# Kernel tuning notes

Hardware: AMD Instinct MI355X
Metric: run time of the kernel (lower is better)

The kernel has to match this reference:

```python
import jax, jax.numpy as jnp
import numpy as np

ALPHA = 1.0
MIN_FEATURE_SIZE = 1.0
SC = 1e-12                      # stabilizer added to first derivatives
EPS_V_FLOOR = 1e-32 / 6.0       # torch.tensor(1e-32 ** 1 / 6) == 1e-32/6 (** binds tighter than /)


def _grad2d(phi, d):
    """Vectorized equivalent of numerical_gradient_2d: central differences in the
    interior, one-sided forward/backward differences at the boundaries."""
    gx = jnp.concatenate([
        (phi[1:2, :] - phi[0:1, :]) / d,           # forward diff at i == 0
        (phi[2:, :] - phi[:-2, :]) / (2.0 * d),    # central diff in interior
        (phi[-1:, :] - phi[-2:-1, :]) / d,         # backward diff at i == H-1
    ], axis=0)
    gy = jnp.concatenate([
        (phi[:, 1:2] - phi[:, 0:1]) / d,
        (phi[:, 2:] - phi[:, :-2]) / (2.0 * d),
        (phi[:, -1:] - phi[:, -2:-1]) / d,
    ], axis=1)
    return gx, gy


def setup_inputs() -> dict:
    key = jax.random.key(0)
    eps = jax.random.normal(key, (4096, 4096), dtype=jnp.float32)
    grid_size = jnp.asarray(0.05, dtype=jnp.float32)
    return {"eps": eps, "grid_size": grid_size}


def reference(eps, grid_size):
    # mirror the field along axis 1 (torch.cat((eps, eps.flip(1)), dim=1)) -> [H, 2W]
    eps = jnp.concatenate([eps, eps[:, ::-1]], axis=1)

    # ls_derivatives: first derivatives (+SC), then second derivatives of those
    eps_x, eps_y = _grad2d(eps, grid_size)
    eps_x = eps_x + SC
    eps_y = eps_y + SC
    eps_xx, eps_xy = _grad2d(eps_x, grid_size)
    _, eps_yy = _grad2d(eps_y, grid_size)

    pi_d = np.pi / (1.1 * MIN_FEATURE_SIZE)
    eps_v = jnp.maximum(jnp.sqrt(eps_x**2 + eps_y**2), EPS_V_FLOOR)
    k = (eps_x**2 * eps_yy - 2.0 * eps_x * eps_y * eps_xy + eps_y**2 * eps_xx) / eps_v**3
    curve_const = jnp.abs(k * jnp.arctan(eps_v / eps)) - pi_d
    return jnp.nansum(ALPHA * jnp.maximum(curve_const, 0.0) * grid_size**2)
```

## Files before the change

### kernel.cpp

```cpp
#include <hip/hip_runtime.h>
#include <math.h>


#define BLOCK_X 256
#define ROWS_PER 32

typedef float f32x2 __attribute__((ext_vector_type(2)));

__device__ __forceinline__ f32x2 mk2(float a, float b) { f32x2 v; v.x = a; v.y = b; return v; }
__device__ __forceinline__ f32x2 sp2(float a) { return mk2(a, a); }

#if __has_builtin(__builtin_elementwise_fma)
__device__ __forceinline__ f32x2 fma2(f32x2 a, f32x2 b, f32x2 c) { return __builtin_elementwise_fma(a, b, c); }
#else
__device__ __forceinline__ f32x2 fma2(f32x2 a, f32x2 b, f32x2 c) { return mk2(fmaf(a.x, b.x, c.x), fmaf(a.y, b.y, c.y)); }
#endif
#if __has_builtin(__builtin_elementwise_max)
__device__ __forceinline__ f32x2 max2(f32x2 a, f32x2 b) { return __builtin_elementwise_max(a, b); }
#else
__device__ __forceinline__ f32x2 max2(f32x2 a, f32x2 b) { return mk2(fmaxf(a.x, b.x), fmaxf(a.y, b.y)); }
#endif
__device__ __forceinline__ f32x2 abs2(f32x2 a) { return mk2(fabsf(a.x), fabsf(a.y)); }


__device__ __forceinline__ float fast_atan_ratio(float v, float c, float rv)
{
    const float rc = __builtin_amdgcn_rcpf(c);
    const float q  = v * rc;
    const float iq = c * rv;
    const bool  big = fabsf(q) > 1.0f;
    const float t  = big ? iq : q;
    const float s  = t * t;
    float p = fmaf(s, -0.01172120f, 0.05265332f);
    p = fmaf(s, p, -0.11643287f);
    p = fmaf(s, p,  0.19354346f);
    p = fmaf(s, p, -0.33262347f);
    p = fmaf(s, p,  0.99997726f);
    const float at = p * t;
    const float hp = copysignf(1.57079632679f, q);
    return big ? (hp - at) : at;
}

__device__ __forceinline__ f32x2 fast_atan_ratio2(f32x2 v, f32x2 c, f32x2 rvv)
{
    const f32x2 rc = mk2(__builtin_amdgcn_rcpf(c.x), __builtin_amdgcn_rcpf(c.y));
    const f32x2 q  = v * rc;
    const f32x2 iq = c * rvv;
    const bool big0 = fabsf(q.x) > 1.0f, big1 = fabsf(q.y) > 1.0f;
    const f32x2 t = mk2(big0 ? iq.x : q.x, big1 ? iq.y : q.y);
    const f32x2 s = t * t;
    f32x2 p = fma2(s, sp2(-0.01172120f), sp2(0.05265332f));
    p = fma2(s, p, sp2(-0.11643287f));
    p = fma2(s, p, sp2( 0.19354346f));
    p = fma2(s, p, sp2(-0.33262347f));
    p = fma2(s, p, sp2( 0.99997726f));
    const f32x2 at = p * t;
    const float hp0 = copysignf(1.57079632679f, q.x);
    const float hp1 = copysignf(1.57079632679f, q.y);
    return mk2(big0 ? (hp0 - at.x) : at.x, big1 ? (hp1 - at.y) : at.y);
}

template<bool XE>
__device__ __forceinline__ void load6(const float* __restrict__ rowp, int j0,
                                      bool left, bool right,
                                      f32x2& m, f32x2& c, f32x2& p)
{
    c = *reinterpret_cast<const f32x2*>(rowp + j0);
    if (XE) {
        const float* ma = rowp + (left  ? j0 : j0 - 2);
        const float* pa = rowp + (right ? j0 : j0 + 2);
        m = *reinterpret_cast<const f32x2*>(ma);
        p = *reinterpret_cast<const f32x2*>(pa);
        if (left)  m = mk2(c.x, c.x);
        if (right) p = mk2(c.y, c.x);
    } else {
        m = *reinterpret_cast<const f32x2*>(rowp + j0 - 2);
        p = *reinterpret_cast<const f32x2*>(rowp + j0 + 2);
    }
}

template<bool XE>
__device__ __forceinline__ f32x2 strip_packed(
    const float* __restrict__ eps, int Wn, int i0, int j0,
    bool left, bool right, float rd2, f32x2 syjv, f32x2 symv)
{
    const f32x2 SC2    = sp2(1e-12f);
    const float FLOORV = (float)(1e-32 / 6.0);
    const float pi_d   = 3.14159265358979323846f / 1.1f;
    const f32x2 rd2v   = sp2(rd2);
    const f32x2 sxy    = syjv * rd2;

    const float* r0 = eps + (size_t)(i0 - 2) * (size_t)Wn;
    const f32x2 Ac = *reinterpret_cast<const f32x2*>(r0 + j0);
    f32x2 Bm, Bc, Bp, Cm, Cc, Cp, Dm, Dc, Dp, Em, Ec, Ep;
    load6<XE>(r0 + (size_t)Wn,     j0, left, right, Bm, Bc, Bp);
    load6<XE>(r0 + (size_t)2 * Wn, j0, left, right, Cm, Cc, Cp);
    load6<XE>(r0 + (size_t)3 * Wn, j0, left, right, Dm, Dc, Dp);
    load6<XE>(r0 + (size_t)4 * Wn, j0, left, right, Em, Ec, Ep);
    const float* pr = r0 + (size_t)5 * Wn;

    f32x2 xm1 = fma2(Cc - Ac, rd2v, SC2);
    f32x2 gc0 = Dc - Bc;
    f32x2 x0  = fma2(gc0, rd2v, SC2);
    f32x2 gc1 = Ec - Cc;
    f32x2 xp1 = fma2(gc1, rd2v, SC2);

    f32x2 acc = sp2(0.0f);
    #pragma unroll 4
    for (int r = 0; r < ROWS_PER; ++r) {
        f32x2 Fm, Fc, Fp;
        load6<XE>(pr, j0, left, right, Fm, Fc, Fp);
        pr += Wn;

        const f32x2 gc2 = Fc - Dc;
        const f32x2 x2v = fma2(gc2, rd2v, SC2);

        const f32x2 ex  = x0;
        const f32x2 exx = (xp1 - xm1) * rd2;
        const f32x2 Cl1 = mk2(Cm.y, Cc.x), Cr1 = mk2(Cc.y, Cp.x);
        const f32x2 ey  = fma2(Cr1 - Cl1, syjv, SC2);
        f32x2 eyw = fma2(Cc - Cm, symv, SC2);
        const f32x2 eye = fma2(Cp - Cc, rd2v, SC2);
        if (XE) { if (left) eyw.x = ey.x; }
        const f32x2 eyy = (eye - eyw) * syjv;
        const f32x2 Gm = Dm - Bm, Gp = Dp - Bp;
        const f32x2 exyL = mk2(Gm.y, gc0.x), exyR = mk2(gc0.y, Gp.x);
        const f32x2 exy = (exyR - exyL) * sxy;

        const f32x2 t1 = ex * ex, t2 = ey * ey;
        f32x2 num = t1 * eyy;
        num = fma2(t2, exx, num);
        num = fma2((ex * ey) * -2.0f, exy, num);
        const f32x2 ssum = t1 + t2;
        const f32x2 rvv = mk2(__builtin_amdgcn_rsqf(ssum.x),
                              __builtin_amdgcn_rsqf(ssum.y));
        f32x2 evv = ssum * rvv;
        evv = max2(evv, sp2(FLOORV));
        const f32x2 k   = num * (rvv * rvv) * rvv;
        const f32x2 at  = fast_atan_ratio2(evv, Cc, rvv);
        const f32x2 cc  = abs2(k * at) - sp2(pi_d);
        acc = acc + max2(cc, sp2(0.0f));

        xm1 = x0; x0 = xp1; xp1 = x2v; gc0 = gc1; gc1 = gc2;
        Bm = Cm; Bp = Cp;
        Cm = Dm; Cc = Dc; Cp = Dp;
        Dm = Em; Dc = Ec; Dp = Ep;
        Em = Fm; Ec = Fc; Ep = Fp;
    }
    (void)Bc;
    return acc;
}

__device__ float strip_scalar_yb(const float* __restrict__ eps, int Hn, int Wn,
                                 int i0, int j, float rd, float rd2)
{
    const float SC     = 1e-12f;
    const float FLOORV = (float)(1e-32 / 6.0);
    const float pi_d   = 3.14159265358979323846f / 1.1f;

    const int jm  = (j > 0) ? j - 1 : 0;
    const int jmm = (j > 1) ? j - 2 : 0;
    const int jp = j + 1, jpp = j + 2;
    const int cjp  = (jp  < Wn) ? jp  : (2 * Wn - 1 - jp);
    const int cjpp = (jpp < Wn) ? jpp : (2 * Wn - 1 - jpp);
    const bool jz = (j == 0);
    const float syj = jz ? rd : rd2;
    const float sym = (jm == 0) ? rd : rd2;

    auto rp = [&](int t) -> const float* {
        int tt = t < 0 ? 0 : t;
        tt = tt > Hn - 1 ? Hn - 1 : tt;
        return eps + (size_t)tt * (size_t)Wn;
    };

    float a2 = rp(i0 - 2)[j],   a1 = rp(i0 - 1)[j],  a0 = rp(i0)[j];
    float b1 = rp(i0 + 1)[j],   b2 = rp(i0 + 2)[j];
    float wN = rp(i0 - 1)[jm],  w0 = rp(i0)[jm],     wS = rp(i0 + 1)[jm];
    float eN = rp(i0 - 1)[cjp], e0 = rp(i0)[cjp],    eS = rp(i0 + 1)[cjp];
    float ww = rp(i0)[jmm],     ee = rp(i0)[cjpp];

    float acc = 0.0f;
    #pragma unroll 4
    for (int r = 0; r < ROWS_PER; ++r) {
        const int i = i0 + r;
        const float* q3 = rp(i + 3);
        const float* q2 = rp(i + 2);
        const float* q1 = rp(i + 1);
        const float nb2 = q3[j], nwS = q2[jm], neS = q2[cjp];
        const float nww = q1[jmm], nee = q1[cjpp];

        const bool itop = (i == 0), ibot = (i == Hn - 1);
        const float sxi = (itop || ibot) ? rd : rd2;
        const float sxm = (i == 1) ? rd : rd2;
        const float sxp = (i == Hn - 2) ? rd : rd2;

        const float ex = fmaf(b1 - a1, sxi, SC);
        const float ey = fmaf(e0 - w0, syj, SC);
        float exn = fmaf(a0 - a2, sxm, SC);
        float exs = fmaf(b2 - a0, sxp, SC);
        if (itop) exn = ex;
        if (ibot) exs = ex;
        const float exx = (exs - exn) * sxi;
        float eyw = fmaf(a0 - ww, sym, SC);
        const float eye = fmaf(ee - a0, rd2, SC);
        if (jz) eyw = ey;
        const float eyy = (eye - eyw) * syj;
        const float exy = ((eS - eN) - (wS - wN)) * (sxi * syj);

        const float t1 = ex * ex, t2 = ey * ey;
        float num = t1 * eyy;
        num = fmaf(t2, exx, num);
        num = fmaf(-2.0f * (ex * ey), exy, num);
        const float ssum = t1 + t2;
        const float rv = __builtin_amdgcn_rsqf(ssum);
        float ev = ssum * rv;
        ev = fmaxf(ev, FLOORV);
        const float k  = num * (rv * rv) * rv;
        const float at = fast_atan_ratio(ev, a0, rv);
        const float ccv = fabsf(k * at) - pi_d;
        float contrib = fmaxf(ccv, 0.0f);
        if (i >= Hn) contrib = 0.0f;
        acc += contrib;

        a2 = a1; a1 = a0; a0 = b1; b1 = b2; b2 = nb2;
        wN = w0; w0 = wS; wS = nwS;
        eN = e0; e0 = eS; eS = neS;
        ww = nww; ee = nee;
    }
    return acc;
}

__global__ __launch_bounds__(BLOCK_X, 4) void curve_partial_kernel(
    const float* __restrict__ eps, const float* __restrict__ gs,
    double* __restrict__ partial, int Hn, int Wn)
{
    const int tx = threadIdx.x;
    const int j0 = (blockIdx.x * BLOCK_X + tx) * 2;
    const int i0 = blockIdx.y * ROWS_PER;
    const float d   = gs[0];
    const float rd  = 1.0f / d;
    const float rd2 = 0.5f * rd;
    const bool left  = (j0 == 0);
    const bool right = (j0 + 2 == Wn);

    const bool yint = (i0 >= 2) && (i0 + ROWS_PER + 2 < Hn);

    f32x2 accv;
    if (yint) {
        const f32x2 syjv = left ? mk2(rd,  rd2) : sp2(rd2);
        const f32x2 symv = left ? mk2(rd2, rd ) : sp2(rd2);
        const bool xe = (blockIdx.x == 0) || (blockIdx.x == gridDim.x - 1);
        accv = xe
            ? strip_packed<true >(eps, Wn, i0, j0, left, right, rd2, syjv, symv)
            : strip_packed<false>(eps, Wn, i0, j0, left, right, rd2, syjv, symv);
    } else {
        accv.x = strip_scalar_yb(eps, Hn, Wn, i0, j0,     rd, rd2);
        accv.y = strip_scalar_yb(eps, Hn, Wn, i0, j0 + 1, rd, rd2);
    }

    double acc = (double)accv.x + (double)accv.y;
    #pragma unroll
    for (int off = 32; off > 0; off >>= 1)
        acc += __shfl_down(acc, off, 64);
    __shared__ double lds[BLOCK_X / 64];
    const int lane = tx & 63, wv = tx >> 6;
    if (lane == 0) lds[wv] = acc;
    __syncthreads();
    if (tx == 0) {
        partial[blockIdx.y * gridDim.x + blockIdx.x] =
            lds[0] + lds[1] + lds[2] + lds[3];
    }
}

__global__ __launch_bounds__(256) void curve_finish_kernel(
    const double* __restrict__ partial, int n,
    const float* __restrict__ gs, float* __restrict__ out)
{
    const int tx = threadIdx.x;
    double acc = 0.0;
    for (int idx = tx; idx < n; idx += 256) acc += partial[idx];
    #pragma unroll
    for (int off = 32; off > 0; off >>= 1)
        acc += __shfl_down(acc, off, 64);
    __shared__ double lds[4];
    const int lane = tx & 63, wv = tx >> 6;
    if (lane == 0) lds[wv] = acc;
    __syncthreads();
    if (tx == 0) {
        const double dd = (double)gs[0];
        out[0] = (float)((lds[0] + lds[1] + lds[2] + lds[3]) * 2.0 * dd * dd);
    }
}

extern "C" void kernel_launch(void* const* d_in, const int* in_sizes, int n_in,
                              void* d_out, int out_size, void* d_ws, size_t ws_size,
                              hipStream_t stream) {
    const float* eps = (const float*)d_in[0];
    const float* gs  = (const float*)d_in[1];
    float* out = (float*)d_out;

    const int n = in_sizes[0];
    int Wn = (int)(sqrt((double)n) + 0.5);
    int Hn = n / Wn;

    const int gx = Wn / (BLOCK_X * 2);
    const int gy = (Hn + ROWS_PER - 1) / ROWS_PER;
    const int nb = gx * gy;
    double* partial = (double*)d_ws;

    curve_partial_kernel<<<dim3(gx, gy), BLOCK_X, 0, stream>>>(eps, gs, partial, Hn, Wn);
    curve_finish_kernel<<<1, 256, 0, stream>>>(partial, nb, gs, out);
}
```

Measured before the change: 108.6 us.

## Process four columns per thread with 16-byte loads and branch-light atan

```diff
diff --git a/kernel.cpp b/kernel.cpp
--- a/kernel.cpp
+++ b/kernel.cpp
@@ -3,9 +3,10 @@
 
 
 #define BLOCK_X 256
-#define ROWS_PER 32
+#define ROWS_PER 16
 
 typedef float f32x2 __attribute__((ext_vector_type(2)));
+typedef float f32x4 __attribute__((ext_vector_type(4)));
 
 __device__ __forceinline__ f32x2 mk2(float a, float b) { f32x2 v; v.x = a; v.y = b; return v; }
 __device__ __forceinline__ f32x2 sp2(float a) { return mk2(a, a); }
@@ -17,11 +18,49 @@
 #endif
 #if __has_builtin(__builtin_elementwise_max)
 __device__ __forceinline__ f32x2 max2(f32x2 a, f32x2 b) { return __builtin_elementwise_max(a, b); }
+__device__ __forceinline__ f32x2 min2(f32x2 a, f32x2 b) { return __builtin_elementwise_min(a, b); }
 #else
 __device__ __forceinline__ f32x2 max2(f32x2 a, f32x2 b) { return mk2(fmaxf(a.x, b.x), fmaxf(a.y, b.y)); }
+__device__ __forceinline__ f32x2 min2(f32x2 a, f32x2 b) { return mk2(fminf(a.x, b.x), fminf(a.y, b.y)); }
 #endif
 __device__ __forceinline__ f32x2 abs2(f32x2 a) { return mk2(fabsf(a.x), fabsf(a.y)); }
-
+__device__ __forceinline__ f32x2 rcp2(f32x2 a) { return mk2(__builtin_amdgcn_rcpf(a.x), __builtin_amdgcn_rcpf(a.y)); }
+
+struct V4 { f32x2 lo, hi; };
+__device__ __forceinline__ V4 mkv(f32x2 lo, f32x2 hi) { V4 r; r.lo = lo; r.hi = hi; return r; }
+__device__ __forceinline__ V4 splat4(float x) { return mkv(sp2(x), sp2(x)); }
+__device__ __forceinline__ V4 add4(V4 a, V4 b) { return mkv(a.lo + b.lo, a.hi + b.hi); }
+__device__ __forceinline__ V4 sub4(V4 a, V4 b) { return mkv(a.lo - b.lo, a.hi - b.hi); }
+__device__ __forceinline__ V4 mul4(V4 a, V4 b) { return mkv(a.lo * b.lo, a.hi * b.hi); }
+__device__ __forceinline__ V4 muls(V4 a, float s) { return mkv(a.lo * s, a.hi * s); }
+__device__ __forceinline__ V4 fma4(V4 a, V4 b, V4 c) { return mkv(fma2(a.lo, b.lo, c.lo), fma2(a.hi, b.hi, c.hi)); }
+__device__ __forceinline__ V4 fmas(V4 a, f32x2 s, f32x2 c) { return mkv(fma2(a.lo, s, c), fma2(a.hi, s, c)); }
+__device__ __forceinline__ V4 max4(V4 a, V4 b) { return mkv(max2(a.lo, b.lo), max2(a.hi, b.hi)); }
+__device__ __forceinline__ V4 abs4(V4 a) { return mkv(abs2(a.lo), abs2(a.hi)); }
+
+__device__ __forceinline__ V4 atan4_bl(V4 v, V4 c)
+{
+    V4 a  = abs4(c);
+    V4 mn = mkv(min2(v.lo, a.lo), min2(v.hi, a.hi));
+    V4 mx = mkv(max2(v.lo, a.lo), max2(v.hi, a.hi));
+    V4 r  = mkv(rcp2(mx.lo), rcp2(mx.hi));
+    V4 t  = mul4(mn, r);
+    V4 s  = mul4(t, t);
+    V4 p  = fma4(s, splat4(-0.01172120f), splat4(0.05265332f));
+    p = fma4(s, p, splat4(-0.11643287f));
+    p = fma4(s, p, splat4( 0.19354346f));
+    p = fma4(s, p, splat4(-0.33262347f));
+    p = fma4(s, p, splat4( 0.99997726f));
+    V4 at0 = mul4(p, t);
+    const f32x2 P2 = sp2(1.57079632679f);
+    V4 alt = mkv(P2 - at0.lo, P2 - at0.hi);
+    V4 res;
+    res.lo.x = copysignf((v.lo.x > a.lo.x) ? alt.lo.x : at0.lo.x, c.lo.x);
+    res.lo.y = copysignf((v.lo.y > a.lo.y) ? alt.lo.y : at0.lo.y, c.lo.y);
+    res.hi.x = copysignf((v.hi.x > a.hi.x) ? alt.hi.x : at0.hi.x, c.hi.x);
+    res.hi.y = copysignf((v.hi.y > a.hi.y) ? alt.hi.y : at0.hi.y, c.hi.y);
+    return res;
+}
 
 __device__ __forceinline__ float fast_atan_ratio(float v, float c, float rv)
 {
@@ -41,113 +80,117 @@
     return big ? (hp - at) : at;
 }
 
-__device__ __forceinline__ f32x2 fast_atan_ratio2(f32x2 v, f32x2 c, f32x2 rvv)
-{
-    const f32x2 rc = mk2(__builtin_amdgcn_rcpf(c.x), __builtin_amdgcn_rcpf(c.y));
-    const f32x2 q  = v * rc;
-    const f32x2 iq = c * rvv;
-    const bool big0 = fabsf(q.x) > 1.0f, big1 = fabsf(q.y) > 1.0f;
-    const f32x2 t = mk2(big0 ? iq.x : q.x, big1 ? iq.y : q.y);
-    const f32x2 s = t * t;
-    f32x2 p = fma2(s, sp2(-0.01172120f), sp2(0.05265332f));
-    p = fma2(s, p, sp2(-0.11643287f));
-    p = fma2(s, p, sp2( 0.19354346f));
-    p = fma2(s, p, sp2(-0.33262347f));
-    p = fma2(s, p, sp2( 0.99997726f));
-    const f32x2 at = p * t;
-    const float hp0 = copysignf(1.57079632679f, q.x);
-    const float hp1 = copysignf(1.57079632679f, q.y);
-    return mk2(big0 ? (hp0 - at.x) : at.x, big1 ? (hp1 - at.y) : at.y);
-}
+struct Row { f32x2 m, c0, c1, p; };
 
 template<bool XE>
-__device__ __forceinline__ void load6(const float* __restrict__ rowp, int j0,
-                                      bool left, bool right,
-                                      f32x2& m, f32x2& c, f32x2& p)
-{
-    c = *reinterpret_cast<const f32x2*>(rowp + j0);
+__device__ __forceinline__ void load8(const float* __restrict__ rowp, int j0,
+                                      bool left, bool right, Row& R)
+{
+    const f32x4 cv = *reinterpret_cast<const f32x4*>(rowp + j0);
+    R.c0 = mk2(cv.x, cv.y);
+    R.c1 = mk2(cv.z, cv.w);
     if (XE) {
         const float* ma = rowp + (left  ? j0 : j0 - 2);
-        const float* pa = rowp + (right ? j0 : j0 + 2);
-        m = *reinterpret_cast<const f32x2*>(ma);
-        p = *reinterpret_cast<const f32x2*>(pa);
-        if (left)  m = mk2(c.x, c.x);
-        if (right) p = mk2(c.y, c.x);
+        const float* pa = rowp + (right ? j0 : j0 + 4);
+        R.m = *reinterpret_cast<const f32x2*>(ma);
+        R.p = *reinterpret_cast<const f32x2*>(pa);
+        if (left)  R.m = mk2(cv.x, cv.x);
+        if (right) R.p = mk2(cv.w, cv.z);
     } else {
-        m = *reinterpret_cast<const f32x2*>(rowp + j0 - 2);
-        p = *reinterpret_cast<const f32x2*>(rowp + j0 + 2);
+        R.m = *reinterpret_cast<const f32x2*>(rowp + j0 - 2);
+        R.p = *reinterpret_cast<const f32x2*>(rowp + j0 + 4);
     }
 }
 
 template<bool XE>
-__device__ __forceinline__ f32x2 strip_packed(
+__device__ __forceinline__ V4 strip_packed4(
     const float* __restrict__ eps, int Wn, int i0, int j0,
-    bool left, bool right, float rd2, f32x2 syjv, f32x2 symv)
+    bool left, bool right, float rd, float rd2)
 {
     const f32x2 SC2    = sp2(1e-12f);
     const float FLOORV = (float)(1e-32 / 6.0);
     const float pi_d   = 3.14159265358979323846f / 1.1f;
     const f32x2 rd2v   = sp2(rd2);
-    const f32x2 sxy    = syjv * rd2;
+    const float rd2sq  = rd2 * rd2;
+    const f32x2 syj_lo = mk2(left ? rd : rd2, rd2);
+    const f32x2 sym_lo = mk2(rd2, left ? rd : rd2);
+    const f32x2 sxy_lo = syj_lo * rd2;
 
     const float* r0 = eps + (size_t)(i0 - 2) * (size_t)Wn;
-    const f32x2 Ac = *reinterpret_cast<const f32x2*>(r0 + j0);
-    f32x2 Bm, Bc, Bp, Cm, Cc, Cp, Dm, Dc, Dp, Em, Ec, Ep;
-    load6<XE>(r0 + (size_t)Wn,     j0, left, right, Bm, Bc, Bp);
-    load6<XE>(r0 + (size_t)2 * Wn, j0, left, right, Cm, Cc, Cp);
-    load6<XE>(r0 + (size_t)3 * Wn, j0, left, right, Dm, Dc, Dp);
-    load6<XE>(r0 + (size_t)4 * Wn, j0, left, right, Em, Ec, Ep);
+    const f32x4 Acv = *reinterpret_cast<const f32x4*>(r0 + j0);
+    f32x2 Bm, Bp;
+    Row C, D, E;
+    V4 xm1, x0, xp1, gc0, gc1;
+    {
+        Row B;
+        load8<XE>(r0 + (size_t)Wn,     j0, left, right, B);
+        Bm = B.m; Bp = B.p;
+        load8<XE>(r0 + (size_t)2 * Wn, j0, left, right, C);
+        load8<XE>(r0 + (size_t)3 * Wn, j0, left, right, D);
+        load8<XE>(r0 + (size_t)4 * Wn, j0, left, right, E);
+        const V4 Ac   = mkv(mk2(Acv.x, Acv.y), mk2(Acv.z, Acv.w));
+        const V4 Ccen = mkv(C.c0, C.c1);
+        const V4 Bcen = mkv(B.c0, B.c1);
+        const V4 Dcen = mkv(D.c0, D.c1);
+        const V4 Ecen = mkv(E.c0, E.c1);
+        gc0 = sub4(Dcen, Bcen);
+        gc1 = sub4(Ecen, Ccen);
+        xm1 = fmas(sub4(Ccen, Ac), rd2v, SC2);
+        x0  = fmas(gc0, rd2v, SC2);
+        xp1 = fmas(gc1, rd2v, SC2);
+    }
     const float* pr = r0 + (size_t)5 * Wn;
 
-    f32x2 xm1 = fma2(Cc - Ac, rd2v, SC2);
-    f32x2 gc0 = Dc - Bc;
-    f32x2 x0  = fma2(gc0, rd2v, SC2);
-    f32x2 gc1 = Ec - Cc;
-    f32x2 xp1 = fma2(gc1, rd2v, SC2);
-
-    f32x2 acc = sp2(0.0f);
-    #pragma unroll 4
+    V4 acc = splat4(0.0f);
+    #pragma unroll 2
     for (int r = 0; r < ROWS_PER; ++r) {
-        f32x2 Fm, Fc, Fp;
-        load6<XE>(pr, j0, left, right, Fm, Fc, Fp);
+        Row F;
+        load8<XE>(pr, j0, left, right, F);
         pr += Wn;
 
-        const f32x2 gc2 = Fc - Dc;
-        const f32x2 x2v = fma2(gc2, rd2v, SC2);
-
-        const f32x2 ex  = x0;
-        const f32x2 exx = (xp1 - xm1) * rd2;
-        const f32x2 Cl1 = mk2(Cm.y, Cc.x), Cr1 = mk2(Cc.y, Cp.x);
-        const f32x2 ey  = fma2(Cr1 - Cl1, syjv, SC2);
-        f32x2 eyw = fma2(Cc - Cm, symv, SC2);
-        const f32x2 eye = fma2(Cp - Cc, rd2v, SC2);
-        if (XE) { if (left) eyw.x = ey.x; }
-        const f32x2 eyy = (eye - eyw) * syjv;
-        const f32x2 Gm = Dm - Bm, Gp = Dp - Bp;
-        const f32x2 exyL = mk2(Gm.y, gc0.x), exyR = mk2(gc0.y, Gp.x);
-        const f32x2 exy = (exyR - exyL) * sxy;
-
-        const f32x2 t1 = ex * ex, t2 = ey * ey;
-        f32x2 num = t1 * eyy;
-        num = fma2(t2, exx, num);
-        num = fma2((ex * ey) * -2.0f, exy, num);
-        const f32x2 ssum = t1 + t2;
-        const f32x2 rvv = mk2(__builtin_amdgcn_rsqf(ssum.x),
-                              __builtin_amdgcn_rsqf(ssum.y));
-        f32x2 evv = ssum * rvv;
-        evv = max2(evv, sp2(FLOORV));
-        const f32x2 k   = num * (rvv * rvv) * rvv;
-        const f32x2 at  = fast_atan_ratio2(evv, Cc, rvv);
-        const f32x2 cc  = abs2(k * at) - sp2(pi_d);
-        acc = acc + max2(cc, sp2(0.0f));
-
+        const V4 gc2 = mkv(F.c0 - D.c0, F.c1 - D.c1);
+        const V4 x2v = fmas(gc2, rd2v, SC2);
+
+        const V4 ex  = x0;
+        const V4 exx = muls(sub4(xp1, xm1), rd2);
+
+        const V4 Cl1 = mkv(mk2(C.m.y, C.c0.x), mk2(C.c0.y, C.c1.x));
+        const V4 Cr1 = mkv(Cl1.hi, mk2(C.c1.y, C.p.x));
+        const V4 ey  = mkv(fma2(Cr1.lo - Cl1.lo, syj_lo, SC2),
+                           fma2(Cr1.hi - Cl1.hi, rd2v,   SC2));
+
+        const f32x2 midd  = fma2(C.c1 - C.c0, rd2v, SC2);
+        f32x2 eyw_lo      = fma2(C.c0 - C.m, sym_lo, SC2);
+        if (XE) { if (left) eyw_lo.x = ey.lo.x; }
+        const f32x2 eye_hi = fma2(C.p - C.c1, rd2v, SC2);
+        const V4 eyy = mkv((midd - eyw_lo) * syj_lo, (eye_hi - midd) * rd2);
+
+        const f32x2 Gm = D.m - Bm, Gp = D.p - Bp;
+        const V4 Gl1 = mkv(mk2(Gm.y, gc0.lo.x), mk2(gc0.lo.y, gc0.hi.x));
+        const V4 Gr1 = mkv(Gl1.hi, mk2(gc0.hi.y, Gp.x));
+        const V4 exy = mkv((Gr1.lo - Gl1.lo) * sxy_lo,
+                           (Gr1.hi - Gl1.hi) * rd2sq);
+
+        const V4 t1 = mul4(ex, ex), t2 = mul4(ey, ey);
+        V4 num = mul4(t1, eyy);
+        num = fma4(t2, exx, num);
+        num = fma4(muls(mul4(ex, ey), -2.0f), exy, num);
+        const V4 ssum = add4(t1, t2);
+        const V4 rv = mkv(mk2(__builtin_amdgcn_rsqf(ssum.lo.x),
+                              __builtin_amdgcn_rsqf(ssum.lo.y)),
+                          mk2(__builtin_amdgcn_rsqf(ssum.hi.x),
+                              __builtin_amdgcn_rsqf(ssum.hi.y)));
+        V4 ev = mul4(ssum, rv);
+        ev = max4(ev, splat4(FLOORV));
+        const V4 k  = mul4(mul4(num, mul4(rv, rv)), rv);
+        const V4 at = atan4_bl(ev, mkv(C.c0, C.c1));
+        const V4 cc = sub4(abs4(mul4(k, at)), splat4(pi_d));
+        acc = add4(acc, max4(cc, splat4(0.0f)));
+
+        Bm = C.m; Bp = C.p;
+        C = D; D = E; E = F;
         xm1 = x0; x0 = xp1; xp1 = x2v; gc0 = gc1; gc1 = gc2;
-        Bm = Cm; Bp = Cp;
-        Cm = Dm; Cc = Dc; Cp = Dp;
-        Dm = Em; Dc = Ec; Dp = Ep;
-        Em = Fm; Ec = Fc; Ep = Fp;
-    }
-    (void)Bc;
+    }
     return acc;
 }
 
@@ -235,30 +278,31 @@
     double* __restrict__ partial, int Hn, int Wn)
 {
     const int tx = threadIdx.x;
-    const int j0 = (blockIdx.x * BLOCK_X + tx) * 2;
+    const int j0 = (blockIdx.x * BLOCK_X + tx) * 4;
     const int i0 = blockIdx.y * ROWS_PER;
     const float d   = gs[0];
     const float rd  = 1.0f / d;
     const float rd2 = 0.5f * rd;
     const bool left  = (j0 == 0);
-    const bool right = (j0 + 2 == Wn);
+    const bool right = (j0 + 4 == Wn);
 
     const bool yint = (i0 >= 2) && (i0 + ROWS_PER + 2 < Hn);
 
-    f32x2 accv;
+    V4 accv;
     if (yint) {
-        const f32x2 syjv = left ? mk2(rd,  rd2) : sp2(rd2);
-        const f32x2 symv = left ? mk2(rd2, rd ) : sp2(rd2);
         const bool xe = (blockIdx.x == 0) || (blockIdx.x == gridDim.x - 1);
         accv = xe
-            ? strip_packed<true >(eps, Wn, i0, j0, left, right, rd2, syjv, symv)
-            : strip_packed<false>(eps, Wn, i0, j0, left, right, rd2, syjv, symv);
+            ? strip_packed4<true >(eps, Wn, i0, j0, left, right, rd, rd2)
+            : strip_packed4<false>(eps, Wn, i0, j0, left, right, rd, rd2);
     } else {
-        accv.x = strip_scalar_yb(eps, Hn, Wn, i0, j0,     rd, rd2);
-        accv.y = strip_scalar_yb(eps, Hn, Wn, i0, j0 + 1, rd, rd2);
-    }
-
-    double acc = (double)accv.x + (double)accv.y;
+        accv.lo = mk2(strip_scalar_yb(eps, Hn, Wn, i0, j0,     rd, rd2),
+                      strip_scalar_yb(eps, Hn, Wn, i0, j0 + 1, rd, rd2));
+        accv.hi = mk2(strip_scalar_yb(eps, Hn, Wn, i0, j0 + 2, rd, rd2),
+                      strip_scalar_yb(eps, Hn, Wn, i0, j0 + 3, rd, rd2));
+    }
+
+    double acc = ((double)accv.lo.x + (double)accv.lo.y)
+               + ((double)accv.hi.x + (double)accv.hi.y);
     #pragma unroll
     for (int off = 32; off > 0; off >>= 1)
         acc += __shfl_down(acc, off, 64);
@@ -303,7 +347,7 @@
     int Wn = (int)(sqrt((double)n) + 0.5);
     int Hn = n / Wn;
 
-    const int gx = Wn / (BLOCK_X * 2);
+    const int gx = Wn / (BLOCK_X * 4);
     const int gy = (Hn + ROWS_PER - 1) / ROWS_PER;
     const int nb = gx * gy;
     double* partial = (double*)d_ws;
```

Result: slower. 121.9 us (+12.2%).
